# Kernel optimization log

Measured on AMD Instinct MI355X. Metric: run time of the kernel, lower is better.

## Reference

```python
import jax, jax.numpy as jnp
import numpy as np

C = 10  # cluster_num
EMB = 64

def setup_inputs() -> dict:
    key = jax.random.key(0)
    ks = jax.random.split(key, 12)
    B, N, D = 8, 4096, 1024
    n_classes = 1
    data = jax.random.normal(ks[0], (B, N, D), dtype=jnp.float32)
    labels = jax.random.randint(ks[1], (B, N), 0, C, dtype=jnp.int32)
    s = 0.02
    return {
        "data": data,
        "labels": labels,
        # embedding_net: Conv2d(1024,64,1) == linear on feature dim
        "W1": jax.random.normal(ks[2], (EMB, D), dtype=jnp.float32) * s,
        "b1": jnp.zeros((EMB,), dtype=jnp.float32),
        # attention MLP: Linear(64,32) -> tanh -> Linear(32,1)
        "Wa1": jax.random.normal(ks[3], (32, EMB), dtype=jnp.float32) * s,
        "ba1": jnp.zeros((32,), dtype=jnp.float32),
        "Wa2": jax.random.normal(ks[4], (1, 32), dtype=jnp.float32) * s,
        "ba2": jnp.zeros((1,), dtype=jnp.float32),
        # fc6: Linear(64,32) -> ReLU -> (Dropout eval=identity) -> Linear(32,n_classes)
        "Wf1": jax.random.normal(ks[5], (32, EMB), dtype=jnp.float32) * s,
        "bf1": jnp.zeros((32,), dtype=jnp.float32),
        "Wf2": jax.random.normal(ks[6], (n_classes, 32), dtype=jnp.float32) * s,
        "bf2": jnp.zeros((n_classes,), dtype=jnp.float32),
    }

def _masked_softmax(x, mask):
    # faithful to the module's numeric trick
    x_masked = x * mask + (1.0 - 1.0 / (mask + 1e-5))
    x_max = jnp.max(x_masked, axis=1, keepdims=True)
    x_exp = jnp.exp(x - x_max) * mask
    return x_exp / jnp.sum(x_exp, axis=1, keepdims=True)

def reference(data, labels, W1, b1, Wa1, ba1, Wa2, ba2, Wf1, bf1, Wf2, bf2):
    B, N, D = data.shape
    # per-patch 1x1-conv embed + ReLU: [B,N,64]
    e = jax.nn.relu(jnp.einsum('bnd,ed->bne', data, W1) + b1)
    # ragged per-cluster mean (AdaptiveAvgPool over each cluster's patches)
    seg = (labels.astype(jnp.int32) + jnp.arange(B, dtype=jnp.int32)[:, None] * C).reshape(-1)
    sums = jax.ops.segment_sum(e.reshape(B * N, EMB), seg, num_segments=B * C)
    counts = jax.ops.segment_sum(jnp.ones((B * N,), dtype=jnp.float32), seg, num_segments=B * C)
    sums = sums.reshape(B, C, EMB)
    counts = counts.reshape(B, C)
    mask = (counts > 0).astype(jnp.float32)
    h = sums / jnp.maximum(counts, 1.0)[..., None]  # [B,C,64]
    # attention scores over clusters
    a = jnp.einsum('bce,oe->bco', jnp.tanh(jnp.einsum('bce,he->bch', h, Wa1) + ba1), Wa2) + ba2
    A = _masked_softmax(a[..., 0], mask)  # [B,C]
    M = jnp.einsum('bc,bce->be', A, h)    # [B,64]
    # fc6 (dropout is identity at inference)
    logits = jax.nn.relu(M @ Wf1.T + bf1) @ Wf2.T + bf2
    return logits
```

## Files before the change

kernel.cpp:

```cpp
#include <hip/hip_runtime.h>
#include <stdint.h>

#define NC 10
#define EMB 64
#define DD 1024
#define NP 4096
#define NB 8
#define BP 128
#define NBLK (NB * NP / BP)
#define PPB (NP / BP)
#define KCH 128
#define NCHUNK (DD / KCH)
#define WFRAG_U32 65536

typedef __attribute__((ext_vector_type(4))) float f32x4;
typedef __attribute__((ext_vector_type(8))) short short8;

union FragU {
    uint32_t u[4];
    int4     i;
    short8   s;
};

__global__ __launch_bounds__(256) void prep_wfrag(
    const float* __restrict__ W1, uint32_t* __restrict__ wf)
{
    const int tid  = blockIdx.x * 256 + threadIdx.x;
    const int lane = tid & 63;
    const int hl   = (tid >> 6) & 1;
    const int ct   = (tid >> 7) & 3;
    const int kg   = tid >> 9;
    const int e    = ct * 16 + (lane & 15);
    const int k0   = kg * 32 + (lane >> 4) * 8;
    const float* src = W1 + (size_t)e * DD + k0;

    uint32_t out[4];
#pragma unroll
    for (int q = 0; q < 4; ++q) {
        float x0 = src[2 * q], x1 = src[2 * q + 1];
        uint32_t b0 = __float_as_uint(x0), b1 = __float_as_uint(x1);
        uint32_t h0 = (b0 + 0x7fffu + ((b0 >> 16) & 1u)) >> 16;
        uint32_t h1 = (b1 + 0x7fffu + ((b1 >> 16) & 1u)) >> 16;
        if (hl == 0) {
            out[q] = h0 | (h1 << 16);
        } else {
            float r0 = x0 - __uint_as_float(h0 << 16);
            float r1 = x1 - __uint_as_float(h1 << 16);
            uint32_t c0 = __float_as_uint(r0), c1 = __float_as_uint(r1);
            uint32_t l0 = (c0 + 0x7fffu + ((c0 >> 16) & 1u)) >> 16;
            uint32_t l1 = (c1 + 0x7fffu + ((c1 >> 16) & 1u)) >> 16;
            out[q] = l0 | (l1 << 16);
        }
    }
    *(uint4*)(wf + (size_t)tid * 4) = make_uint4(out[0], out[1], out[2], out[3]);
}

__global__ __launch_bounds__(1024, 4) void embed_mfma(
    const float* __restrict__ data, const int* __restrict__ labels,
    const uint32_t* __restrict__ wf, const float* __restrict__ b1,
    float* __restrict__ psum, float* __restrict__ pcnt, int use_atomic)
{
    __shared__ float csum[NC][EMB];
    __shared__ float ccnt[NC];
    __shared__ int   labs[BP];

    const int t    = threadIdx.x;
    const int lane = t & 63;
    const int w    = t >> 6;
    const int pt   = w >> 1;
    const int ch   = w & 1;
    const int bid  = blockIdx.x;
    const int bag  = bid >> 5;
    const int p0   = (bid & 31) * BP;

    for (int i = t; i < NC * EMB; i += 1024) (&csum[0][0])[i] = 0.f;
    if (t < NC) ccnt[t] = 0.f;
    if (t < BP) labs[t] = labels[bag * NP + p0 + t];
    __syncthreads();

    const float* Ap = data + (size_t)(bag * NP + p0 + pt * 16 + (lane & 15)) * DD
                    + ((lane >> 4) << 3);
    const uint4* Wp = (const uint4*)wf + (size_t)(ch * 256 + lane);

    f32x4 acc[2] = {};
    float4 aA[8], aB[8];

#pragma unroll
    for (int ks = 0; ks < 4; ++ks) {
        aA[2 * ks]     = *(const float4*)(Ap + ks * 32);
        aA[2 * ks + 1] = *(const float4*)(Ap + ks * 32 + 4);
    }

#define PACK_HI(x0, x1) ((__float_as_uint(x1) & 0xffff0000u) | (__float_as_uint(x0) >> 16))
#define SPLIT_KSTEP(ACUR, ks, ahi, alo)                                          \
    {                                                                            \
        const float4 a0 = ACUR[2 * (ks)], a1 = ACUR[2 * (ks) + 1];               \
        ahi.u[0] = PACK_HI(a0.x, a0.y);                                          \
        ahi.u[1] = PACK_HI(a0.z, a0.w);                                          \
        ahi.u[2] = PACK_HI(a1.x, a1.y);                                          \
        ahi.u[3] = PACK_HI(a1.z, a1.w);                                          \
        float r0 = a0.x - __uint_as_float(__float_as_uint(a0.x) & 0xffff0000u);  \
        float r1 = a0.y - __uint_as_float(__float_as_uint(a0.y) & 0xffff0000u);  \
        float r2 = a0.z - __uint_as_float(__float_as_uint(a0.z) & 0xffff0000u);  \
        float r3 = a0.w - __uint_as_float(__float_as_uint(a0.w) & 0xffff0000u);  \
        float r4 = a1.x - __uint_as_float(__float_as_uint(a1.x) & 0xffff0000u);  \
        float r5 = a1.y - __uint_as_float(__float_as_uint(a1.y) & 0xffff0000u);  \
        float r6 = a1.z - __uint_as_float(__float_as_uint(a1.z) & 0xffff0000u);  \
        float r7 = a1.w - __uint_as_float(__float_as_uint(a1.w) & 0xffff0000u);  \
        alo.u[0] = PACK_HI(r0, r1);                                              \
        alo.u[1] = PACK_HI(r2, r3);                                              \
        alo.u[2] = PACK_HI(r4, r5);                                              \
        alo.u[3] = PACK_HI(r6, r7);                                              \
    }

#define CHUNK(c, ACUR, ANEXT)                                                    \
    {                                                                            \
        if ((c) + 1 < NCHUNK) {                                                  \
            _Pragma("unroll")                                                    \
            for (int ks = 0; ks < 4; ++ks) {                                     \
                ANEXT[2 * ks]     = *(const float4*)(Ap + ((c) + 1) * KCH + ks * 32);      \
                ANEXT[2 * ks + 1] = *(const float4*)(Ap + ((c) + 1) * KCH + ks * 32 + 4);  \
            }                                                                    \
        }                                                                        \
        _Pragma("unroll")                                                        \
        for (int ks = 0; ks < 4; ++ks) {                                         \
            FragU ahi, alo;                                                      \
            SPLIT_KSTEP(ACUR, ks, ahi, alo);                                     \
            _Pragma("unroll")                                                    \
            for (int ct2 = 0; ct2 < 2; ++ct2) {                                  \
                FragU bhi, blo;                                                  \
                bhi.i = *(const int4*)&Wp[(size_t)(((c) * 4 + ks) * 512 + ct2 * 128)];       \
                blo.i = *(const int4*)&Wp[(size_t)(((c) * 4 + ks) * 512 + ct2 * 128 + 64)];  \
                acc[ct2] = __builtin_amdgcn_mfma_f32_16x16x32_bf16(ahi.s, bhi.s, acc[ct2], 0, 0, 0); \
                acc[ct2] = __builtin_amdgcn_mfma_f32_16x16x32_bf16(ahi.s, blo.s, acc[ct2], 0, 0, 0); \
                acc[ct2] = __builtin_amdgcn_mfma_f32_16x16x32_bf16(alo.s, bhi.s, acc[ct2], 0, 0, 0); \
            }                                                                    \
        }                                                                        \
    }

    CHUNK(0, aA, aB)
    CHUNK(1, aB, aA)
    CHUNK(2, aA, aB)
    CHUNK(3, aB, aA)
    CHUNK(4, aA, aB)
    CHUNK(5, aB, aA)
    CHUNK(6, aA, aB)
    CHUNK(7, aB, aA)

#pragma unroll
    for (int ct2 = 0; ct2 < 2; ++ct2) {
        const int emb = (2 * ch + ct2) * 16 + (lane & 15);
        const float bb = b1[emb];
#pragma unroll
        for (int r = 0; r < 4; ++r) {
            const int patch = pt * 16 + (lane >> 4) * 4 + r;
            float v = fmaxf(acc[ct2][r] + bb, 0.f);
            atomicAdd(&csum[labs[patch]][emb], v);
        }
    }
    if (t < BP) atomicAdd(&ccnt[labs[t]], 1.0f);
    __syncthreads();

    if (use_atomic) {
        for (int i = t; i < NC * EMB; i += 1024)
            atomicAdd(&psum[(size_t)bag * NC * EMB + i], (&csum[0][0])[i]);
        if (t < NC) atomicAdd(&pcnt[bag * NC + t], ccnt[t]);
    } else {
        for (int i = t; i < NC * EMB; i += 1024)
            psum[(size_t)bid * NC * EMB + i] = (&csum[0][0])[i];
        if (t < NC) pcnt[bid * NC + t] = ccnt[t];
    }
}

__global__ __launch_bounds__(256) void head_kernel(
    const float* __restrict__ psum, const float* __restrict__ pcnt, int npb,
    const float* __restrict__ Wa1, const float* __restrict__ ba1,
    const float* __restrict__ Wa2, const float* __restrict__ ba2,
    const float* __restrict__ Wf1, const float* __restrict__ bf1,
    const float* __restrict__ Wf2, const float* __restrict__ bf2,
    float* __restrict__ out)
{
    __shared__ float h[NC][EMB];
    __shared__ float cnt_s[NC];
    __shared__ float mask[NC];
    __shared__ float att[NC][32];
    __shared__ float a_s[NC];
    __shared__ float A_s[NC];
    __shared__ float M_s[EMB];
    __shared__ float f_s[32];

    const int b = blockIdx.x;
    const int t = threadIdx.x;

    if (t < NC) {
        float s = 0.f;
        for (int pb = 0; pb < npb; ++pb) s += pcnt[(size_t)(b * npb + pb) * NC + t];
        cnt_s[t] = s;
        mask[t]  = s > 0.f ? 1.f : 0.f;
    }
    __syncthreads();
    for (int i = t; i < NC * EMB; i += 256) {
        float s = 0.f;
        for (int pb = 0; pb < npb; ++pb) s += psum[(size_t)(b * npb + pb) * NC * EMB + i];
        (&h[0][0])[i] = s / fmaxf(cnt_s[i >> 6], 1.f);
    }
    __syncthreads();

    for (int task = t; task < NC * 32; task += 256) {
        int c = task >> 5, hh = task & 31;
        float s = ba1[hh];
        for (int e = 0; e < EMB; ++e) s = fmaf(Wa1[hh * EMB + e], h[c][e], s);
        att[c][hh] = tanhf(s);
    }
    __syncthreads();

    if (t < NC) {
        float s = ba2[0];
        for (int hh = 0; hh < 32; ++hh) s = fmaf(Wa2[hh], att[t][hh], s);
        a_s[t] = s;
    }
    __syncthreads();

    if (t == 0) {
        float xmax = -1e30f;
        for (int c = 0; c < NC; ++c) {
            float xm = a_s[c] * mask[c] + (1.0f - 1.0f / (mask[c] + 1e-5f));
            xmax = fmaxf(xmax, xm);
        }
        float ex[NC], ssum = 0.f;
        for (int c = 0; c < NC; ++c) {
            ex[c] = expf(a_s[c] - xmax) * mask[c];
            ssum += ex[c];
        }
        for (int c = 0; c < NC; ++c) A_s[c] = ex[c] / ssum;
    }
    __syncthreads();

    if (t < EMB) {
        float s = 0.f;
        for (int c = 0; c < NC; ++c) s = fmaf(A_s[c], h[c][t], s);
        M_s[t] = s;
    }
    __syncthreads();

    if (t < 32) {
        float s = bf1[t];
        for (int e = 0; e < EMB; ++e) s = fmaf(Wf1[t * EMB + e], M_s[e], s);
        f_s[t] = fmaxf(s, 0.f);
    }
    __syncthreads();

    if (t == 0) {
        float s = bf2[0];
        for (int hh = 0; hh < 32; ++hh) s = fmaf(Wf2[hh], f_s[hh], s);
        out[b] = s;
    }
}

extern "C" void kernel_launch(void* const* d_in, const int* in_sizes, int n_in,
                              void* d_out, int out_size, void* d_ws, size_t ws_size,
                              hipStream_t stream)
{
    const float* data   = (const float*)d_in[0];
    const int*   labels = (const int*)  d_in[1];
    const float* W1     = (const float*)d_in[2];
    const float* b1     = (const float*)d_in[3];
    const float* Wa1    = (const float*)d_in[4];
    const float* ba1    = (const float*)d_in[5];
    const float* Wa2    = (const float*)d_in[6];
    const float* ba2    = (const float*)d_in[7];
    const float* Wf1    = (const float*)d_in[8];
    const float* bf1    = (const float*)d_in[9];
    const float* Wf2    = (const float*)d_in[10];
    const float* bf2    = (const float*)d_in[11];

    uint32_t* wfrag = (uint32_t*)d_ws;
    float* psum = (float*)(wfrag + WFRAG_U32);

    prep_wfrag<<<64, 256, 0, stream>>>(W1, wfrag);

    const size_t need_na = (size_t)WFRAG_U32 * 4 +
                           ((size_t)NBLK * NC * EMB + (size_t)NBLK * NC) * sizeof(float);
    if (ws_size >= need_na) {
        float* pcnt = psum + (size_t)NBLK * NC * EMB;
        embed_mfma<<<NBLK, 1024, 0, stream>>>(data, labels, wfrag, b1, psum, pcnt, 0);
        head_kernel<<<NB, 256, 0, stream>>>(psum, pcnt, PPB, Wa1, ba1, Wa2, ba2,
                                            Wf1, bf1, Wf2, bf2, (float*)d_out);
    } else {
        float* pcnt = psum + (size_t)NB * NC * EMB;
        hipMemsetAsync((void*)psum, 0,
                       (size_t)(NB * NC * EMB + NB * NC) * sizeof(float), stream);
        embed_mfma<<<NBLK, 1024, 0, stream>>>(data, labels, wfrag, b1, psum, pcnt, 1);
        head_kernel<<<NB, 256, 0, stream>>>(psum, pcnt, 1, Wa1, ba1, Wa2, ba2,
                                            Wf1, bf1, Wf2, bf2, (float*)d_out);
    }
}
```

Baseline: 276.2 us.

## Shrink embed blocks to 32 patches, one 16-col tile per wave, drop prefetch

Block size drops from 128 to 32 patches with 512 threads, and each wave now computes a single 16-column embedding tile instead of two. This quadruples the block count, which should give more blocks to spread over the CUs and more waves in flight per CU. The explicit register double-buffered prefetch of A is replaced with a plain per-chunk loop that also loads the B fragments up front. In exchange, each data row is now read by four waves instead of two, so the same input is loaded redundantly more often. The head kernel must also reduce four times as many partial sums, and that loop gets an unroll hint.

```diff
diff --git a/kernel.cpp b/kernel.cpp
--- a/kernel.cpp
+++ b/kernel.cpp
@@ -6,7 +6,7 @@
 #define DD 1024
 #define NP 4096
 #define NB 8
-#define BP 128
+#define BP 32
 #define NBLK (NB * NP / BP)
 #define PPB (NP / BP)
 #define KCH 128
@@ -55,7 +55,7 @@
     *(uint4*)(wf + (size_t)tid * 4) = make_uint4(out[0], out[1], out[2], out[3]);
 }
 
-__global__ __launch_bounds__(1024, 4) void embed_mfma(
+__global__ __launch_bounds__(512, 8) void embed_mfma(
     const float* __restrict__ data, const int* __restrict__ labels,
     const uint32_t* __restrict__ wf, const float* __restrict__ b1,
     float* __restrict__ psum, float* __restrict__ pcnt, int use_atomic)
@@ -67,94 +67,74 @@
     const int t    = threadIdx.x;
     const int lane = t & 63;
     const int w    = t >> 6;
-    const int pt   = w >> 1;
-    const int ch   = w & 1;
+    const int pt   = w >> 2;
+    const int ct   = w & 3;
     const int bid  = blockIdx.x;
-    const int bag  = bid >> 5;
-    const int p0   = (bid & 31) * BP;
-
-    for (int i = t; i < NC * EMB; i += 1024) (&csum[0][0])[i] = 0.f;
+    const int bag  = bid >> 7;
+    const int p0   = (bid & 127) * BP;
+
+    for (int i = t; i < NC * EMB; i += 512) (&csum[0][0])[i] = 0.f;
     if (t < NC) ccnt[t] = 0.f;
     if (t < BP) labs[t] = labels[bag * NP + p0 + t];
     __syncthreads();
 
     const float* Ap = data + (size_t)(bag * NP + p0 + pt * 16 + (lane & 15)) * DD
                     + ((lane >> 4) << 3);
-    const uint4* Wp = (const uint4*)wf + (size_t)(ch * 256 + lane);
-
-    f32x4 acc[2] = {};
-    float4 aA[8], aB[8];
-
-#pragma unroll
-    for (int ks = 0; ks < 4; ++ks) {
-        aA[2 * ks]     = *(const float4*)(Ap + ks * 32);
-        aA[2 * ks + 1] = *(const float4*)(Ap + ks * 32 + 4);
-    }
+    const uint4* Wp = (const uint4*)wf + (size_t)(ct * 128 + lane);
+
+    f32x4 acc = {};
 
 #define PACK_HI(x0, x1) ((__float_as_uint(x1) & 0xffff0000u) | (__float_as_uint(x0) >> 16))
-#define SPLIT_KSTEP(ACUR, ks, ahi, alo)                                          \
-    {                                                                            \
-        const float4 a0 = ACUR[2 * (ks)], a1 = ACUR[2 * (ks) + 1];               \
-        ahi.u[0] = PACK_HI(a0.x, a0.y);                                          \
-        ahi.u[1] = PACK_HI(a0.z, a0.w);                                          \
-        ahi.u[2] = PACK_HI(a1.x, a1.y);                                          \
-        ahi.u[3] = PACK_HI(a1.z, a1.w);                                          \
-        float r0 = a0.x - __uint_as_float(__float_as_uint(a0.x) & 0xffff0000u);  \
-        float r1 = a0.y - __uint_as_float(__float_as_uint(a0.y) & 0xffff0000u);  \
-        float r2 = a0.z - __uint_as_float(__float_as_uint(a0.z) & 0xffff0000u);  \
-        float r3 = a0.w - __uint_as_float(__float_as_uint(a0.w) & 0xffff0000u);  \
-        float r4 = a1.x - __uint_as_float(__float_as_uint(a1.x) & 0xffff0000u);  \
-        float r5 = a1.y - __uint_as_float(__float_as_uint(a1.y) & 0xffff0000u);  \
-        float r6 = a1.z - __uint_as_float(__float_as_uint(a1.z) & 0xffff0000u);  \
-        float r7 = a1.w - __uint_as_float(__float_as_uint(a1.w) & 0xffff0000u);  \
-        alo.u[0] = PACK_HI(r0, r1);                                              \
-        alo.u[1] = PACK_HI(r2, r3);                                              \
-        alo.u[2] = PACK_HI(r4, r5);                                              \
-        alo.u[3] = PACK_HI(r6, r7);                                              \
-    }
-
-#define CHUNK(c, ACUR, ANEXT)                                                    \
-    {                                                                            \
-        if ((c) + 1 < NCHUNK) {                                                  \
-            _Pragma("unroll")                                                    \
-            for (int ks = 0; ks < 4; ++ks) {                                     \
-                ANEXT[2 * ks]     = *(const float4*)(Ap + ((c) + 1) * KCH + ks * 32);      \
-                ANEXT[2 * ks + 1] = *(const float4*)(Ap + ((c) + 1) * KCH + ks * 32 + 4);  \
-            }                                                                    \
-        }                                                                        \
-        _Pragma("unroll")                                                        \
-        for (int ks = 0; ks < 4; ++ks) {                                         \
-            FragU ahi, alo;                                                      \
-            SPLIT_KSTEP(ACUR, ks, ahi, alo);                                     \
-            _Pragma("unroll")                                                    \
-            for (int ct2 = 0; ct2 < 2; ++ct2) {                                  \
-                FragU bhi, blo;                                                  \
-                bhi.i = *(const int4*)&Wp[(size_t)(((c) * 4 + ks) * 512 + ct2 * 128)];       \
-                blo.i = *(const int4*)&Wp[(size_t)(((c) * 4 + ks) * 512 + ct2 * 128 + 64)];  \
-                acc[ct2] = __builtin_amdgcn_mfma_f32_16x16x32_bf16(ahi.s, bhi.s, acc[ct2], 0, 0, 0); \
-                acc[ct2] = __builtin_amdgcn_mfma_f32_16x16x32_bf16(ahi.s, blo.s, acc[ct2], 0, 0, 0); \
-                acc[ct2] = __builtin_amdgcn_mfma_f32_16x16x32_bf16(alo.s, bhi.s, acc[ct2], 0, 0, 0); \
-            }                                                                    \
-        }                                                                        \
-    }
-
-    CHUNK(0, aA, aB)
-    CHUNK(1, aB, aA)
-    CHUNK(2, aA, aB)
-    CHUNK(3, aB, aA)
-    CHUNK(4, aA, aB)
-    CHUNK(5, aB, aA)
-    CHUNK(6, aA, aB)
-    CHUNK(7, aB, aA)
-
-#pragma unroll
-    for (int ct2 = 0; ct2 < 2; ++ct2) {
-        const int emb = (2 * ch + ct2) * 16 + (lane & 15);
+
+    for (int c = 0; c < NCHUNK; ++c) {
+        float4 a[8];
+        uint4  bw[8];
+#pragma unroll
+        for (int ks = 0; ks < 4; ++ks) {
+            a[2 * ks]     = *(const float4*)(Ap + c * KCH + ks * 32);
+            a[2 * ks + 1] = *(const float4*)(Ap + c * KCH + ks * 32 + 4);
+        }
+#pragma unroll
+        for (int ks = 0; ks < 4; ++ks) {
+            bw[2 * ks]     = Wp[(size_t)((c * 4 + ks) * 512)];
+            bw[2 * ks + 1] = Wp[(size_t)((c * 4 + ks) * 512 + 64)];
+        }
+#pragma unroll
+        for (int ks = 0; ks < 4; ++ks) {
+            const float4 a0 = a[2 * ks], a1 = a[2 * ks + 1];
+            FragU ahi, alo;
+            ahi.u[0] = PACK_HI(a0.x, a0.y);
+            ahi.u[1] = PACK_HI(a0.z, a0.w);
+            ahi.u[2] = PACK_HI(a1.x, a1.y);
+            ahi.u[3] = PACK_HI(a1.z, a1.w);
+            float r0 = a0.x - __uint_as_float(__float_as_uint(a0.x) & 0xffff0000u);
+            float r1 = a0.y - __uint_as_float(__float_as_uint(a0.y) & 0xffff0000u);
+            float r2 = a0.z - __uint_as_float(__float_as_uint(a0.z) & 0xffff0000u);
+            float r3 = a0.w - __uint_as_float(__float_as_uint(a0.w) & 0xffff0000u);
+            float r4 = a1.x - __uint_as_float(__float_as_uint(a1.x) & 0xffff0000u);
+            float r5 = a1.y - __uint_as_float(__float_as_uint(a1.y) & 0xffff0000u);
+            float r6 = a1.z - __uint_as_float(__float_as_uint(a1.z) & 0xffff0000u);
+            float r7 = a1.w - __uint_as_float(__float_as_uint(a1.w) & 0xffff0000u);
+            alo.u[0] = PACK_HI(r0, r1);
+            alo.u[1] = PACK_HI(r2, r3);
+            alo.u[2] = PACK_HI(r4, r5);
+            alo.u[3] = PACK_HI(r6, r7);
+            FragU bhi, blo;
+            bhi.i = *(const int4*)&bw[2 * ks];
+            blo.i = *(const int4*)&bw[2 * ks + 1];
+            acc = __builtin_amdgcn_mfma_f32_16x16x32_bf16(ahi.s, bhi.s, acc, 0, 0, 0);
+            acc = __builtin_amdgcn_mfma_f32_16x16x32_bf16(ahi.s, blo.s, acc, 0, 0, 0);
+            acc = __builtin_amdgcn_mfma_f32_16x16x32_bf16(alo.s, bhi.s, acc, 0, 0, 0);
+        }
+    }
+
+    {
+        const int emb = ct * 16 + (lane & 15);
         const float bb = b1[emb];
 #pragma unroll
         for (int r = 0; r < 4; ++r) {
             const int patch = pt * 16 + (lane >> 4) * 4 + r;
-            float v = fmaxf(acc[ct2][r] + bb, 0.f);
+            float v = fmaxf(acc[r] + bb, 0.f);
             atomicAdd(&csum[labs[patch]][emb], v);
         }
     }
@@ -162,11 +142,11 @@
     __syncthreads();
 
     if (use_atomic) {
-        for (int i = t; i < NC * EMB; i += 1024)
+        for (int i = t; i < NC * EMB; i += 512)
             atomicAdd(&psum[(size_t)bag * NC * EMB + i], (&csum[0][0])[i]);
         if (t < NC) atomicAdd(&pcnt[bag * NC + t], ccnt[t]);
     } else {
-        for (int i = t; i < NC * EMB; i += 1024)
+        for (int i = t; i < NC * EMB; i += 512)
             psum[(size_t)bid * NC * EMB + i] = (&csum[0][0])[i];
         if (t < NC) pcnt[bid * NC + t] = ccnt[t];
     }
@@ -201,6 +181,7 @@
     __syncthreads();
     for (int i = t; i < NC * EMB; i += 256) {
         float s = 0.f;
+#pragma unroll 8
         for (int pb = 0; pb < npb; ++pb) s += psum[(size_t)(b * npb + pb) * NC * EMB + i];
         (&h[0][0])[i] = s / fmaxf(cnt_s[i >> 6], 1.f);
     }
@@ -283,14 +264,14 @@
                            ((size_t)NBLK * NC * EMB + (size_t)NBLK * NC) * sizeof(float);
     if (ws_size >= need_na) {
         float* pcnt = psum + (size_t)NBLK * NC * EMB;
-        embed_mfma<<<NBLK, 1024, 0, stream>>>(data, labels, wfrag, b1, psum, pcnt, 0);
+        embed_mfma<<<NBLK, 512, 0, stream>>>(data, labels, wfrag, b1, psum, pcnt, 0);
         head_kernel<<<NB, 256, 0, stream>>>(psum, pcnt, PPB, Wa1, ba1, Wa2, ba2,
                                             Wf1, bf1, Wf2, bf2, (float*)d_out);
     } else {
         float* pcnt = psum + (size_t)NB * NC * EMB;
         hipMemsetAsync((void*)psum, 0,
                        (size_t)(NB * NC * EMB + NB * NC) * sizeof(float), stream);
-        embed_mfma<<<NBLK, 1024, 0, stream>>>(data, labels, wfrag, b1, psum, pcnt, 1);
+        embed_mfma<<<NBLK, 512, 0, stream>>>(data, labels, wfrag, b1, psum, pcnt, 1);
         head_kernel<<<NB, 256, 0, stream>>>(psum, pcnt, 1, Wa1, ba1, Wa2, ba2,
                                             Wf1, bf1, Wf2, bf2, (float*)d_out);
     }
```

Measured after the change: 295.2 us. 1.07x slower.
